# Performance work log

Hardware: AMD Instinct MI355X
Metric: run time of the kernel (lower is better)

## Reference

```python
import jax, jax.numpy as jnp
import numpy as np

ALPHA = 0.1
MARGIN = 1.0
SLOPE = 0.2  # LeakyReLU negative_slope
OFFSET = 1.0e6

def leaky(x):
    return jnp.where(x >= 0, x, SLOPE * x)

def _xavier(key, shape, gain=np.sqrt(2.0)):
    fan_out, fan_in = shape[0], shape[1]
    std = gain * np.sqrt(2.0 / (fan_in + fan_out))
    return jax.random.normal(key, shape, dtype=jnp.float32) * std

def setup_inputs() -> dict:
    key = jax.random.key(0)
    ks = jax.random.split(key, 8)
    B, F, T, D, H = 32768, 128, 32, 16, 10
    return {
        "X": jax.random.normal(ks[0], (B, F), dtype=jnp.float32),
        "affine_weights": jax.random.normal(ks[1], (T, F, D), dtype=jnp.float32),
        "W0": _xavier(ks[2], (H, D)),
        "W1": _xavier(ks[3], (H, H)),
        "W2": _xavier(ks[4], (H, H)),
        "W3": _xavier(ks[5], (H, H)),
        "Wh": _xavier(ks[6], (T, H)),
        "bh": jnp.zeros((T,), dtype=jnp.float32),
    }

def reference(X, affine_weights, W0, W1, W2, W3, Wh, bh):
    T = affine_weights.shape[0]
    # goad_transforms: x_trans [B, trans_dim, n_trans]; labels[b,t] = t (implicit)
    x_trans = jnp.einsum('bn,ant->bta', X, affine_weights)
    # ConvNet encoder, kernel_size=1 convs == per-position channel matmuls
    h = jnp.einsum('od,bdt->bot', W0, x_trans)
    for W in (W1, W2, W3):
        h = jnp.einsum('od,bdt->bot', W, leaky(h))
    rep = h                                   # [B, H, T]
    # head: LeakyReLU + Conv1d(H->T, bias=True)
    pred = jnp.einsum('oh,bht->bot', Wh, leaky(rep)) + bh[None, :, None]  # [B, T, T]
    batch_rep = jnp.transpose(rep, (0, 2, 1))  # [B, T, H]
    # CrossEntropy(reduction='none') with labels[b,t]=t -> -diag of log_softmax over class dim
    logp = jax.nn.log_softmax(pred, axis=1)
    loss_ce = -jnp.diagonal(logp, axis1=1, axis2=2)          # [B, T]
    # triplet center loss
    means = jnp.mean(batch_rep, axis=0)                       # [T, H]
    res = jnp.sum((batch_rep[:, :, None, :] - means[None, None, :, :]) ** 2, axis=-1)  # [B,T,T]
    pos = jnp.diagonal(res, axis1=1, axis2=2)                 # [B, T]
    neg = jnp.min(res + jnp.eye(T, dtype=res.dtype) * OFFSET, axis=-1)  # [B, T]
    loss_tc = jnp.mean(jnp.maximum(pos + MARGIN - neg, 0.0))  # scalar
    loss = jnp.mean(ALPHA * loss_tc + loss_ce, axis=1)        # [B]
    return batch_rep, loss
```

## Files before the change

kernel.cpp:

```cpp
#include <hip/hip_runtime.h>

typedef __attribute__((ext_vector_type(8))) short bf16x8;
typedef __attribute__((ext_vector_type(4))) float f32x4;

#define BTOT 32768
#define FDIM 128
#define TDIM 32
#define DDIM 16
#define HDIM 10
#define CDIM 320
#define ALPHA_C 0.1f
#define MARGIN_C 1.0f
#define SLOPE_C 0.2f
#define OFFSET_C 1.0e6f

#define WS_A0BF 0
#define WS_MEAN 20480
#define WS_TC   20800
#define WS_CE   20864

#define R2OFF 23552
#define LDS_TOTAL (R2OFF + 21760)
#define YSROW 92
#define MPROW 81

__device__ __forceinline__ float leaky(float x) { return fmaxf(x, SLOPE_C * x); }

__device__ __forceinline__ unsigned short f2bf(float f) {
    unsigned int u = __float_as_uint(f);
    u += 0x7fffu + ((u >> 16) & 1u);
    return (unsigned short)(u >> 16);
}

__global__ void prep_kernel(const float* __restrict__ aw, const float* __restrict__ W0,
                            unsigned short* __restrict__ a0bf) {
    int idx = blockIdx.x * blockDim.x + threadIdx.x;
    if (idx >= CDIM * FDIM) return;
    int c = idx >> 7, n = idx & 127;
    int t = c / HDIM, o = c - t * HDIM;
    const float* a = aw + ((size_t)t * FDIM + n) * DDIM;
    const float* w = W0 + o * DDIM;
    float s = 0.f;
#pragma unroll
    for (int d = 0; d < DDIM; ++d) s += a[d] * w[d];
    a0bf[idx] = f2bf(s);
}

__global__ __launch_bounds__(256, 3) void gemm0_fused(
    const float* __restrict__ X, const unsigned short* __restrict__ a0bf,
    const float* __restrict__ W1, const float* __restrict__ W2,
    const float* __restrict__ W3, const float* __restrict__ Wh,
    const float* __restrict__ bh,
    float* __restrict__ rep, float* __restrict__ ce_acc,
    float* __restrict__ mean_acc)
{
    __shared__ __align__(16) char ldsbuf[LDS_TOTAL];
    unsigned short (*xs)[136]  = (unsigned short (*)[136])ldsbuf;
    float* ysf = (float*)ldsbuf;
    unsigned short (*a0s)[136] = (unsigned short (*)[136])(ldsbuf + R2OFF);
    float* mpartf = (float*)(ldsbuf + R2OFF);

    int tid = threadIdx.x;
    int bchunk = blockIdx.x >> 2, cchunk = blockIdx.x & 3;
    int b0 = bchunk * 64, c0 = cchunk * 80;

#pragma unroll
    for (int k = 0; k < 8; ++k) {
        int idx = tid + k * 256;
        int row = idx >> 5, col4 = idx & 31;
        float4 v = reinterpret_cast<const float4*>(X + (size_t)(b0 + row) * FDIM)[col4];
        unsigned pk0, pk1;
        asm("v_cvt_pk_bf16_f32 %0, %1, %2" : "=v"(pk0) : "v"(v.x), "v"(v.y));
        asm("v_cvt_pk_bf16_f32 %0, %1, %2" : "=v"(pk1) : "v"(v.z), "v"(v.w));
        uint2 pk; pk.x = pk0; pk.y = pk1;
        *reinterpret_cast<uint2*>(&xs[row][col4 * 4]) = pk;
    }
#pragma unroll
    for (int k = 0; k < 5; ++k) {
        int idx = tid + k * 256;
        int row = idx >> 4, j = idx & 15;
        uint4 v = reinterpret_cast<const uint4*>(a0bf + (size_t)(c0 + row) * FDIM)[j];
        *reinterpret_cast<uint4*>(&a0s[row][j * 8]) = v;
    }
    __syncthreads();

    int lane = tid & 63, w = __builtin_amdgcn_readfirstlane(tid >> 6);
    int r16 = lane & 15, g = lane >> 4;
    bf16x8 af[4];
#pragma unroll
    for (int s = 0; s < 4; ++s)
        af[s] = *reinterpret_cast<const bf16x8*>(&xs[w * 16 + r16][s * 32 + g * 8]);
    __syncthreads();

#pragma unroll
    for (int ct = 0; ct < 5; ++ct) {
        f32x4 acc = {0.f, 0.f, 0.f, 0.f};
#pragma unroll
        for (int s = 0; s < 4; ++s) {
            bf16x8 bfrag = *reinterpret_cast<const bf16x8*>(&a0s[ct * 16 + r16][s * 32 + g * 8]);
            acc = __builtin_amdgcn_mfma_f32_16x16x32_bf16(af[s], bfrag, acc, 0, 0, 0);
        }
        int c = ct * 16 + r16;
        int cpad = c + c / 10;
        int ybase = (w * 16 + g * 4) * YSROW + cpad;
#pragma unroll
        for (int r = 0; r < 4; ++r) ysf[ybase + r * YSROW] = acc[r];
    }
    __syncthreads();

    int t8 = tid & 7, bl0 = tid >> 3;
    int t = cchunk * 8 + t8;
    float mgg[HDIM];
#pragma unroll
    for (int o = 0; o < HDIM; ++o) mgg[o] = 0.f;

#pragma unroll
    for (int p = 0; p < 2; ++p) {
        int bl = bl0 + p * 32;
        const float* yrow = ysf + bl * YSROW + t8 * 11;
        float h[HDIM], lh[HDIM], gg[HDIM];
#pragma unroll
        for (int q = 0; q < HDIM; ++q) h[q] = yrow[q];
#pragma unroll
        for (int o = 0; o < HDIM; ++o) lh[o] = leaky(h[o]);
#pragma unroll
        for (int o = 0; o < HDIM; ++o) { float s = 0.f;
#pragma unroll
            for (int i = 0; i < HDIM; ++i) s += W1[o * HDIM + i] * lh[i]; gg[o] = s; }
#pragma unroll
        for (int o = 0; o < HDIM; ++o) lh[o] = leaky(gg[o]);
#pragma unroll
        for (int o = 0; o < HDIM; ++o) { float s = 0.f;
#pragma unroll
            for (int i = 0; i < HDIM; ++i) s += W2[o * HDIM + i] * lh[i]; h[o] = s; }
#pragma unroll
        for (int o = 0; o < HDIM; ++o) lh[o] = leaky(h[o]);
#pragma unroll
        for (int o = 0; o < HDIM; ++o) { float s = 0.f;
#pragma unroll
            for (int i = 0; i < HDIM; ++i) s += W3[o * HDIM + i] * lh[i]; gg[o] = s; }

        float* rp = rep + (size_t)(b0 + bl) * CDIM + c0 + t8 * 10;
#pragma unroll
        for (int q = 0; q < 5; ++q) {
            float2 v; v.x = gg[2 * q]; v.y = gg[2 * q + 1];
            reinterpret_cast<float2*>(rp)[q] = v;
        }
#pragma unroll
        for (int o = 0; o < HDIM; ++o) mgg[o] += gg[o];

#pragma unroll
        for (int o = 0; o < HDIM; ++o) lh[o] = leaky(gg[o]);
        float m = -1e30f, se = 0.f, pt = 0.f;
#pragma unroll
        for (int o = 0; o < TDIM; ++o) {
            float s = bh[o];
#pragma unroll
            for (int i = 0; i < HDIM; ++i) s += Wh[o * HDIM + i] * lh[i];
            pt = (o == t) ? s : pt;
            float d = s - m;
            float e = __expf(-fabsf(d));
            float ra = d > 0.f ? e : 1.f;
            float rb = d > 0.f ? 1.f : e;
            se = se * ra + rb;
            m = fmaxf(m, s);
        }
        float ce = m + __logf(se) - pt;
        ce += __shfl_xor(ce, 1, 64);
        ce += __shfl_xor(ce, 2, 64);
        ce += __shfl_xor(ce, 4, 64);
        if (t8 == 0) atomicAdd(&ce_acc[b0 + bl], ce);
    }

#pragma unroll
    for (int o = 0; o < HDIM; ++o) mpartf[bl0 * MPROW + t8 * HDIM + o] = mgg[o];
    __syncthreads();
    if (tid < 80) {
        float s = 0.f;
#pragma unroll
        for (int r = 0; r < 32; ++r) s += mpartf[r * MPROW + tid];
        atomicAdd(&mean_acc[c0 + tid], s);
    }
}

__global__ __launch_bounds__(256) void tc_kernel(const float* __restrict__ rep,
    const float* __restrict__ mean_acc, float* __restrict__ tc_sum)
{
    __shared__ float tile[32][CDIM];
    __shared__ float mm[CDIM];
    __shared__ float msq[TDIM];
    __shared__ float wpart[4];
    int tid = threadIdx.x;
    int b0 = blockIdx.x * 32;

    for (int i = tid; i < CDIM; i += 256) mm[i] = mean_acc[i] * (1.f / BTOT);
    const float4* src = reinterpret_cast<const float4*>(rep + (size_t)b0 * CDIM);
#pragma unroll
    for (int k = 0; k < 10; ++k) {
        int idx = tid + k * 256;
        int row = idx / 80, col4 = idx - row * 80;
        *reinterpret_cast<float4*>(&tile[row][col4 * 4]) = src[idx];
    }
    __syncthreads();
    if (tid < TDIM) {
        float s = 0.f;
#pragma unroll
        for (int h = 0; h < HDIM; ++h) { float v = mm[tid * HDIM + h]; s += v * v; }
        msq[tid] = s;
    }
    __syncthreads();

    int t = tid & 31, bg = tid >> 5;
    float rv[4][HDIM], rsq[4];
#pragma unroll
    for (int j = 0; j < 4; ++j) {
        const float* rp = &tile[bg * 4 + j][t * HDIM];
        float s = 0.f;
#pragma unroll
        for (int q = 0; q < 5; ++q) {
            float2 v = reinterpret_cast<const float2*>(rp)[q];
            rv[j][2 * q] = v.x; rv[j][2 * q + 1] = v.y;
            s += v.x * v.x + v.y * v.y;
        }
        rsq[j] = s;
    }
    float pos[4], neg[4];
#pragma unroll
    for (int j = 0; j < 4; ++j) { pos[j] = 0.f; neg[j] = 1e30f; }
#pragma unroll 4
    for (int c = 0; c < TDIM; ++c) {
        float m0[HDIM];
#pragma unroll
        for (int q = 0; q < 5; ++q) {
            float2 v = reinterpret_cast<const float2*>(&mm[c * HDIM])[q];
            m0[2 * q] = v.x; m0[2 * q + 1] = v.y;
        }
        float mq = msq[c];
        bool isT = (c == t);
#pragma unroll
        for (int j = 0; j < 4; ++j) {
            float dot = 0.f;
#pragma unroll
            for (int h = 0; h < HDIM; ++h) dot += rv[j][h] * m0[h];
            float s = rsq[j] - 2.f * dot + mq;
            if (isT) pos[j] = s;
            float s2 = isT ? s + OFFSET_C : s;
            neg[j] = fminf(neg[j], s2);
        }
    }
    float hs = 0.f;
#pragma unroll
    for (int j = 0; j < 4; ++j) hs += fmaxf(pos[j] + MARGIN_C - neg[j], 0.f);
#pragma unroll
    for (int m = 1; m < 64; m <<= 1) hs += __shfl_xor(hs, m, 64);
    int lane = tid & 63, w = tid >> 6;
    if (lane == 0) wpart[w] = hs;
    __syncthreads();
    if (tid == 0) atomicAdd(tc_sum, wpart[0] + wpart[1] + wpart[2] + wpart[3]);
}

__global__ void final_kernel(const float* __restrict__ ce_acc,
                             const float* __restrict__ tc_sum, float* __restrict__ loss)
{
    int b = blockIdx.x * blockDim.x + threadIdx.x;
    if (b < BTOT)
        loss[b] = ALPHA_C * (tc_sum[0] * (1.f / ((float)BTOT * TDIM)))
                + ce_acc[b] * (1.f / TDIM);
}

extern "C" void kernel_launch(void* const* d_in, const int* in_sizes, int n_in,
                              void* d_out, int out_size, void* d_ws, size_t ws_size,
                              hipStream_t stream) {
    const float* X  = (const float*)d_in[0];
    const float* aw = (const float*)d_in[1];
    const float* W0 = (const float*)d_in[2];
    const float* W1 = (const float*)d_in[3];
    const float* W2 = (const float*)d_in[4];
    const float* W3 = (const float*)d_in[5];
    const float* Wh = (const float*)d_in[6];
    const float* bh = (const float*)d_in[7];
    float* ws = (float*)d_ws;
    unsigned short* a0bf = (unsigned short*)(ws + WS_A0BF);
    float* mean_acc = ws + WS_MEAN;
    float* tc_sum   = ws + WS_TC;
    float* ce_acc   = ws + WS_CE;
    float* out_rep = (float*)d_out;
    float* loss = out_rep + (size_t)BTOT * TDIM * HDIM;

    hipMemsetAsync(mean_acc, 0, (384 + BTOT) * sizeof(float), stream);
    prep_kernel<<<(CDIM * FDIM) / 256, 256, 0, stream>>>(aw, W0, a0bf);
    gemm0_fused<<<2048, 256, 0, stream>>>(X, a0bf, W1, W2, W3, Wh, bh,
                                          out_rep, ce_acc, mean_acc);
    tc_kernel<<<BTOT / 32, 256, 0, stream>>>(out_rep, mean_acc, tc_sum);
    final_kernel<<<BTOT / 256, 256, 0, stream>>>(ce_acc, tc_sum, loss);
}
```

Measured before the change: 90.83 us.

## Run encoder layers and head on MFMA with lane-shuffle fragment chaining

Rewrites the fused kernel so the three 10x10 encoder layers and the 32-way head run as zero-padded bf16 MFMA ops instead of scalar FMA loops. Intermediate activations are passed between MFMAs through cross-lane shuffles rather than an LDS staging tile. The A0 weight is padded to 16 outputs per transform, each block now covers 32 batch rows across all transforms, and the per-row CE atomics are replaced by one atomic per row. This targets the scalar ALU cost of the small dense layers and the LDS round trip. In exchange it computes the hidden layers in bf16, which lowers precision, and wastes MFMA work on padding.

```diff
diff --git a/kernel.cpp b/kernel.cpp
--- a/kernel.cpp
+++ b/kernel.cpp
@@ -14,15 +14,10 @@
 #define SLOPE_C 0.2f
 #define OFFSET_C 1.0e6f
 
-#define WS_A0BF 0
-#define WS_MEAN 20480
-#define WS_TC   20800
-#define WS_CE   20864
-
-#define R2OFF 23552
-#define LDS_TOTAL (R2OFF + 21760)
-#define YSROW 92
-#define MPROW 81
+#define WS_A0P  0
+#define WS_MEAN 32768
+#define WS_TC   33088
+#define WS_CE   33152
 
 __device__ __forceinline__ float leaky(float x) { return fmaxf(x, SLOPE_C * x); }
 
@@ -32,154 +27,184 @@
     return (unsigned short)(u >> 16);
 }
 
+__device__ __forceinline__ f32x4 mfma32(bf16x8 a, bf16x8 b, f32x4 c) {
+    return __builtin_amdgcn_mfma_f32_16x16x32_bf16(a, b, c, 0, 0, 0);
+}
+
+__device__ __forceinline__ void leaky_pack(f32x4 v, unsigned& p0, unsigned& p1) {
+    float a0 = leaky(v[0]), a1 = leaky(v[1]), a2 = leaky(v[2]), a3 = leaky(v[3]);
+    asm("v_cvt_pk_bf16_f32 %0, %1, %2" : "=v"(p0) : "v"(a0), "v"(a1));
+    asm("v_cvt_pk_bf16_f32 %0, %1, %2" : "=v"(p1) : "v"(a2), "v"(a3));
+}
+
+__device__ __forceinline__ bf16x8 build_bfrag(unsigned p0, unsigned p1, int g, int r16) {
+    int s0 = ((2 * g) * 16 + r16) & 63;
+    int s1 = ((2 * g + 1) * 16 + r16) & 63;
+    unsigned w0 = (unsigned)__shfl((int)p0, s0, 64);
+    unsigned w1 = (unsigned)__shfl((int)p1, s0, 64);
+    unsigned w2 = (unsigned)__shfl((int)p0, s1, 64);
+    unsigned w3 = (unsigned)__shfl((int)p1, s1, 64);
+    unsigned zm = (g < 2) ? 0xFFFFFFFFu : 0u;
+    union { unsigned u[4]; bf16x8 v; } r;
+    r.u[0] = w0 & zm; r.u[1] = w1 & zm; r.u[2] = w2 & zm; r.u[3] = w3 & zm;
+    return r.v;
+}
+
 __global__ void prep_kernel(const float* __restrict__ aw, const float* __restrict__ W0,
-                            unsigned short* __restrict__ a0bf) {
+                            unsigned short* __restrict__ a0p) {
     int idx = blockIdx.x * blockDim.x + threadIdx.x;
-    if (idx >= CDIM * FDIM) return;
-    int c = idx >> 7, n = idx & 127;
-    int t = c / HDIM, o = c - t * HDIM;
-    const float* a = aw + ((size_t)t * FDIM + n) * DDIM;
-    const float* w = W0 + o * DDIM;
-    float s = 0.f;
-#pragma unroll
-    for (int d = 0; d < DDIM; ++d) s += a[d] * w[d];
-    a0bf[idx] = f2bf(s);
-}
-
-__global__ __launch_bounds__(256, 3) void gemm0_fused(
-    const float* __restrict__ X, const unsigned short* __restrict__ a0bf,
+    if (idx >= 65536) return;
+    int n = idx & 127, o = (idx >> 7) & 15, t = idx >> 11;
+    unsigned short r = 0;
+    if (o < 10) {
+        const float* a = aw + ((size_t)t * FDIM + n) * DDIM;
+        const float* w = W0 + o * DDIM;
+        float s = 0.f;
+#pragma unroll
+        for (int d = 0; d < DDIM; ++d) s += a[d] * w[d];
+        r = f2bf(s);
+    }
+    a0p[idx] = r;
+}
+
+__global__ __launch_bounds__(256, 4) void gemm0_fused(
+    const float* __restrict__ X, const unsigned short* __restrict__ a0p,
     const float* __restrict__ W1, const float* __restrict__ W2,
     const float* __restrict__ W3, const float* __restrict__ Wh,
     const float* __restrict__ bh,
     float* __restrict__ rep, float* __restrict__ ce_acc,
     float* __restrict__ mean_acc)
 {
-    __shared__ __align__(16) char ldsbuf[LDS_TOTAL];
-    unsigned short (*xs)[136]  = (unsigned short (*)[136])ldsbuf;
-    float* ysf = (float*)ldsbuf;
-    unsigned short (*a0s)[136] = (unsigned short (*)[136])(ldsbuf + R2OFF);
-    float* mpartf = (float*)(ldsbuf + R2OFF);
+    __shared__ unsigned short xs[32][136];
+    __shared__ unsigned short w1x[16][32], w2x[16][32], w3x[16][32], whx[32][32];
+    __shared__ float mred[2][32][12];
 
     int tid = threadIdx.x;
-    int bchunk = blockIdx.x >> 2, cchunk = blockIdx.x & 3;
-    int b0 = bchunk * 64, c0 = cchunk * 80;
-
-#pragma unroll
-    for (int k = 0; k < 8; ++k) {
+    int b0 = blockIdx.x * 32;
+
+#pragma unroll
+    for (int k = 0; k < 4; ++k) {
         int idx = tid + k * 256;
         int row = idx >> 5, col4 = idx & 31;
         float4 v = reinterpret_cast<const float4*>(X + (size_t)(b0 + row) * FDIM)[col4];
-        unsigned pk0, pk1;
-        asm("v_cvt_pk_bf16_f32 %0, %1, %2" : "=v"(pk0) : "v"(v.x), "v"(v.y));
-        asm("v_cvt_pk_bf16_f32 %0, %1, %2" : "=v"(pk1) : "v"(v.z), "v"(v.w));
-        uint2 pk; pk.x = pk0; pk.y = pk1;
+        unsigned p0, p1;
+        asm("v_cvt_pk_bf16_f32 %0, %1, %2" : "=v"(p0) : "v"(v.x), "v"(v.y));
+        asm("v_cvt_pk_bf16_f32 %0, %1, %2" : "=v"(p1) : "v"(v.z), "v"(v.w));
+        uint2 pk; pk.x = p0; pk.y = p1;
         *reinterpret_cast<uint2*>(&xs[row][col4 * 4]) = pk;
     }
 #pragma unroll
-    for (int k = 0; k < 5; ++k) {
-        int idx = tid + k * 256;
-        int row = idx >> 4, j = idx & 15;
-        uint4 v = reinterpret_cast<const uint4*>(a0bf + (size_t)(c0 + row) * FDIM)[j];
-        *reinterpret_cast<uint4*>(&a0s[row][j * 8]) = v;
+    for (int k = 0; k < 2; ++k) {
+        int i = tid + k * 256;
+        int o = i >> 5, kk = i & 31;
+        bool in10 = (o < 10 && kk < 10);
+        w1x[o][kk] = in10 ? f2bf(W1[o * 10 + kk]) : (unsigned short)0;
+        w2x[o][kk] = in10 ? f2bf(W2[o * 10 + kk]) : (unsigned short)0;
+        w3x[o][kk] = in10 ? f2bf(W3[o * 10 + kk]) : (unsigned short)0;
+    }
+#pragma unroll
+    for (int k = 0; k < 4; ++k) {
+        int i = tid + k * 256;
+        int o = i >> 5, kk = i & 31;
+        whx[o][kk] = (kk < 10) ? f2bf(Wh[o * 10 + kk]) : (unsigned short)0;
     }
     __syncthreads();
 
     int lane = tid & 63, w = __builtin_amdgcn_readfirstlane(tid >> 6);
     int r16 = lane & 15, g = lane >> 4;
-    bf16x8 af[4];
+    int bsub = w >> 1, thalf = w & 1;
+    int bglob = b0 + bsub * 16 + r16;
+
+    bf16x8 xf[4];
 #pragma unroll
     for (int s = 0; s < 4; ++s)
-        af[s] = *reinterpret_cast<const bf16x8*>(&xs[w * 16 + r16][s * 32 + g * 8]);
-    __syncthreads();
-
-#pragma unroll
-    for (int ct = 0; ct < 5; ++ct) {
-        f32x4 acc = {0.f, 0.f, 0.f, 0.f};
-#pragma unroll
-        for (int s = 0; s < 4; ++s) {
-            bf16x8 bfrag = *reinterpret_cast<const bf16x8*>(&a0s[ct * 16 + r16][s * 32 + g * 8]);
-            acc = __builtin_amdgcn_mfma_f32_16x16x32_bf16(af[s], bfrag, acc, 0, 0, 0);
+        xf[s] = *reinterpret_cast<const bf16x8*>(&xs[bsub * 16 + r16][s * 32 + g * 8]);
+
+    bf16x8 w1f = *reinterpret_cast<const bf16x8*>(&w1x[r16][g * 8]);
+    bf16x8 w2f = *reinterpret_cast<const bf16x8*>(&w2x[r16][g * 8]);
+    bf16x8 w3f = *reinterpret_cast<const bf16x8*>(&w3x[r16][g * 8]);
+    bf16x8 whAf = *reinterpret_cast<const bf16x8*>(&whx[r16][g * 8]);
+    bf16x8 whBf = *reinterpret_cast<const bf16x8*>(&whx[16 + r16][g * 8]);
+    f32x4 bhA, bhB;
+#pragma unroll
+    for (int r = 0; r < 4; ++r) { bhA[r] = bh[g * 4 + r]; bhB[r] = bh[16 + g * 4 + r]; }
+    const f32x4 zero4 = {0.f, 0.f, 0.f, 0.f};
+
+    float ce_local = 0.f;
+
+    for (int tt4 = 0; tt4 < 4; ++tt4) {
+#pragma unroll
+        for (int q = 0; q < 4; ++q) {
+            int t = thalf * 16 + tt4 * 4 + q;
+            const bf16x8* ap = reinterpret_cast<const bf16x8*>(
+                a0p + ((size_t)t * 16 + r16) * 128);
+            f32x4 acc = zero4;
+#pragma unroll
+            for (int s = 0; s < 4; ++s)
+                acc = mfma32(ap[s * 4 + g], xf[s], acc);
+
+            unsigned p0, p1;
+            leaky_pack(acc, p0, p1);
+            bf16x8 bf = build_bfrag(p0, p1, g, r16);
+            f32x4 d1 = mfma32(w1f, bf, zero4);
+            leaky_pack(d1, p0, p1);
+            bf = build_bfrag(p0, p1, g, r16);
+            f32x4 d2 = mfma32(w2f, bf, zero4);
+            leaky_pack(d2, p0, p1);
+            bf = build_bfrag(p0, p1, g, r16);
+            f32x4 d3 = mfma32(w3f, bf, zero4);
+
+            float* rp = rep + (size_t)bglob * CDIM + t * HDIM + g * 4;
+            if (g < 2) {
+                float2 v0; v0.x = d3[0]; v0.y = d3[1];
+                float2 v1; v1.x = d3[2]; v1.y = d3[3];
+                reinterpret_cast<float2*>(rp)[0] = v0;
+                reinterpret_cast<float2*>(rp)[1] = v1;
+            } else if (g == 2) {
+                float2 v0; v0.x = d3[0]; v0.y = d3[1];
+                reinterpret_cast<float2*>(rp)[0] = v0;
+            }
+
+            float m0 = d3[0], m1 = d3[1], m2 = d3[2], m3 = d3[3];
+#pragma unroll
+            for (int msk = 1; msk < 16; msk <<= 1) {
+                m0 += __shfl_xor(m0, msk, 64);
+                m1 += __shfl_xor(m1, msk, 64);
+                m2 += __shfl_xor(m2, msk, 64);
+                m3 += __shfl_xor(m3, msk, 64);
+            }
+            if (r16 == 0 && g < 3) {
+                float4 mv; mv.x = m0; mv.y = m1; mv.z = m2; mv.w = m3;
+                *reinterpret_cast<float4*>(&mred[bsub][t][g * 4]) = mv;
+            }
+
+            leaky_pack(d3, p0, p1);
+            bf = build_bfrag(p0, p1, g, r16);
+            f32x4 pA = mfma32(whAf, bf, bhA);
+            f32x4 pB = mfma32(whBf, bf, bhB);
+
+            float mx = fmaxf(fmaxf(fmaxf(pA[0], pA[1]), fmaxf(pA[2], pA[3])),
+                             fmaxf(fmaxf(pB[0], pB[1]), fmaxf(pB[2], pB[3])));
+            mx = fmaxf(mx, __shfl_xor(mx, 16, 64));
+            mx = fmaxf(mx, __shfl_xor(mx, 32, 64));
+            float se = __expf(pA[0] - mx) + __expf(pA[1] - mx) +
+                       __expf(pA[2] - mx) + __expf(pA[3] - mx) +
+                       __expf(pB[0] - mx) + __expf(pB[1] - mx) +
+                       __expf(pB[2] - mx) + __expf(pB[3] - mx);
+            se += __shfl_xor(se, 16, 64);
+            se += __shfl_xor(se, 32, 64);
+            float lse = mx + __logf(se);
+            float pr = thalf ? pB[q] : pA[q];
+            float ptv = __shfl(pr, tt4 * 16 + r16, 64);
+            ce_local += lse - ptv;
         }
-        int c = ct * 16 + r16;
-        int cpad = c + c / 10;
-        int ybase = (w * 16 + g * 4) * YSROW + cpad;
-#pragma unroll
-        for (int r = 0; r < 4; ++r) ysf[ybase + r * YSROW] = acc[r];
-    }
-    __syncthreads();
-
-    int t8 = tid & 7, bl0 = tid >> 3;
-    int t = cchunk * 8 + t8;
-    float mgg[HDIM];
-#pragma unroll
-    for (int o = 0; o < HDIM; ++o) mgg[o] = 0.f;
-
-#pragma unroll
-    for (int p = 0; p < 2; ++p) {
-        int bl = bl0 + p * 32;
-        const float* yrow = ysf + bl * YSROW + t8 * 11;
-        float h[HDIM], lh[HDIM], gg[HDIM];
-#pragma unroll
-        for (int q = 0; q < HDIM; ++q) h[q] = yrow[q];
-#pragma unroll
-        for (int o = 0; o < HDIM; ++o) lh[o] = leaky(h[o]);
-#pragma unroll
-        for (int o = 0; o < HDIM; ++o) { float s = 0.f;
-#pragma unroll
-            for (int i = 0; i < HDIM; ++i) s += W1[o * HDIM + i] * lh[i]; gg[o] = s; }
-#pragma unroll
-        for (int o = 0; o < HDIM; ++o) lh[o] = leaky(gg[o]);
-#pragma unroll
-        for (int o = 0; o < HDIM; ++o) { float s = 0.f;
-#pragma unroll
-            for (int i = 0; i < HDIM; ++i) s += W2[o * HDIM + i] * lh[i]; h[o] = s; }
-#pragma unroll
-        for (int o = 0; o < HDIM; ++o) lh[o] = leaky(h[o]);
-#pragma unroll
-        for (int o = 0; o < HDIM; ++o) { float s = 0.f;
-#pragma unroll
-            for (int i = 0; i < HDIM; ++i) s += W3[o * HDIM + i] * lh[i]; gg[o] = s; }
-
-        float* rp = rep + (size_t)(b0 + bl) * CDIM + c0 + t8 * 10;
-#pragma unroll
-        for (int q = 0; q < 5; ++q) {
-            float2 v; v.x = gg[2 * q]; v.y = gg[2 * q + 1];
-            reinterpret_cast<float2*>(rp)[q] = v;
-        }
-#pragma unroll
-        for (int o = 0; o < HDIM; ++o) mgg[o] += gg[o];
-
-#pragma unroll
-        for (int o = 0; o < HDIM; ++o) lh[o] = leaky(gg[o]);
-        float m = -1e30f, se = 0.f, pt = 0.f;
-#pragma unroll
-        for (int o = 0; o < TDIM; ++o) {
-            float s = bh[o];
-#pragma unroll
-            for (int i = 0; i < HDIM; ++i) s += Wh[o * HDIM + i] * lh[i];
-            pt = (o == t) ? s : pt;
-            float d = s - m;
-            float e = __expf(-fabsf(d));
-            float ra = d > 0.f ? e : 1.f;
-            float rb = d > 0.f ? 1.f : e;
-            se = se * ra + rb;
-            m = fmaxf(m, s);
-        }
-        float ce = m + __logf(se) - pt;
-        ce += __shfl_xor(ce, 1, 64);
-        ce += __shfl_xor(ce, 2, 64);
-        ce += __shfl_xor(ce, 4, 64);
-        if (t8 == 0) atomicAdd(&ce_acc[b0 + bl], ce);
-    }
-
-#pragma unroll
-    for (int o = 0; o < HDIM; ++o) mpartf[bl0 * MPROW + t8 * HDIM + o] = mgg[o];
-    __syncthreads();
-    if (tid < 80) {
-        float s = 0.f;
-#pragma unroll
-        for (int r = 0; r < 32; ++r) s += mpartf[r * MPROW + tid];
-        atomicAdd(&mean_acc[c0 + tid], s);
+    }
+
+    if (g == 0) atomicAdd(&ce_acc[bglob], ce_local);
+    __syncthreads();
+    for (int i = tid; i < TDIM * HDIM; i += 256) {
+        int t = i / 10, o = i - t * 10;
+        atomicAdd(&mean_acc[i], mred[0][t][o] + mred[1][t][o]);
     }
 }
 
@@ -280,7 +305,7 @@
     const float* Wh = (const float*)d_in[6];
     const float* bh = (const float*)d_in[7];
     float* ws = (float*)d_ws;
-    unsigned short* a0bf = (unsigned short*)(ws + WS_A0BF);
+    unsigned short* a0p = (unsigned short*)(ws + WS_A0P);
     float* mean_acc = ws + WS_MEAN;
     float* tc_sum   = ws + WS_TC;
     float* ce_acc   = ws + WS_CE;
@@ -288,9 +313,9 @@
     float* loss = out_rep + (size_t)BTOT * TDIM * HDIM;
 
     hipMemsetAsync(mean_acc, 0, (384 + BTOT) * sizeof(float), stream);
-    prep_kernel<<<(CDIM * FDIM) / 256, 256, 0, stream>>>(aw, W0, a0bf);
-    gemm0_fused<<<2048, 256, 0, stream>>>(X, a0bf, W1, W2, W3, Wh, bh,
-                                          out_rep, ce_acc, mean_acc);
+    prep_kernel<<<256, 256, 0, stream>>>(aw, W0, a0p);
+    gemm0_fused<<<BTOT / 32, 256, 0, stream>>>(X, a0p, W1, W2, W3, Wh, bh,
+                                               out_rep, ce_acc, mean_acc);
     tc_kernel<<<BTOT / 32, 256, 0, stream>>>(out_rep, mean_acc, tc_sum);
     final_kernel<<<BTOT / 256, 256, 0, stream>>>(ce_acc, tc_sum, loss);
 }
```

After: 102.9 us. 13.3% more time.

## Move CE head into tc kernel, split mean reduction, restructure gemm0 tiling

Applied to the files above, without the earlier changes.

The classification head and cross-entropy move out of the gemm0 kernel into the triplet-center kernel, which already holds rep in LDS. The CE sums are then written directly per sample, so the atomics and the large memset go away. The column mean is now computed by a separate kernel that rereads rep. Gemm0 now uses 32-row blocks over half the transforms each, reads padded A0 fragments straight from global memory instead of staging them in LDS, and raises occupancy to 4 blocks per CU. The cost is an extra pass over rep for the mean and more global loads of A0.

```diff
diff --git a/kernel.cpp b/kernel.cpp
--- a/kernel.cpp
+++ b/kernel.cpp
@@ -14,15 +14,12 @@
 #define SLOPE_C 0.2f
 #define OFFSET_C 1.0e6f
 
-#define WS_A0BF 0
-#define WS_MEAN 20480
-#define WS_TC   20800
-#define WS_CE   20864
-
-#define R2OFF 23552
-#define LDS_TOTAL (R2OFF + 21760)
-#define YSROW 92
-#define MPROW 81
+#define WS_A0P  0
+#define WS_MEAN 32768
+#define WS_TC   33088
+#define WS_CE   33152
+
+#define YSROW 163
 
 __device__ __forceinline__ float leaky(float x) { return fmaxf(x, SLOPE_C * x); }
 
@@ -32,95 +29,96 @@
     return (unsigned short)(u >> 16);
 }
 
+__device__ __forceinline__ f32x4 mfma32(bf16x8 a, bf16x8 b, f32x4 c) {
+    return __builtin_amdgcn_mfma_f32_16x16x32_bf16(a, b, c, 0, 0, 0);
+}
+
 __global__ void prep_kernel(const float* __restrict__ aw, const float* __restrict__ W0,
-                            unsigned short* __restrict__ a0bf) {
+                            unsigned short* __restrict__ a0p) {
     int idx = blockIdx.x * blockDim.x + threadIdx.x;
-    if (idx >= CDIM * FDIM) return;
-    int c = idx >> 7, n = idx & 127;
-    int t = c / HDIM, o = c - t * HDIM;
-    const float* a = aw + ((size_t)t * FDIM + n) * DDIM;
-    const float* w = W0 + o * DDIM;
-    float s = 0.f;
-#pragma unroll
-    for (int d = 0; d < DDIM; ++d) s += a[d] * w[d];
-    a0bf[idx] = f2bf(s);
-}
-
-__global__ __launch_bounds__(256, 3) void gemm0_fused(
-    const float* __restrict__ X, const unsigned short* __restrict__ a0bf,
+    if (idx >= 65536) return;
+    int n = idx & 127, o = (idx >> 7) & 15, t = idx >> 11;
+    unsigned short r = 0;
+    if (o < 10) {
+        const float* a = aw + ((size_t)t * FDIM + n) * DDIM;
+        const float* w = W0 + o * DDIM;
+        float s = 0.f;
+#pragma unroll
+        for (int d = 0; d < DDIM; ++d) s += a[d] * w[d];
+        r = f2bf(s);
+    }
+    a0p[idx] = r;
+}
+
+__global__ __launch_bounds__(256, 4) void gemm0_fused(
+    const float* __restrict__ X, const unsigned short* __restrict__ a0p,
     const float* __restrict__ W1, const float* __restrict__ W2,
-    const float* __restrict__ W3, const float* __restrict__ Wh,
-    const float* __restrict__ bh,
-    float* __restrict__ rep, float* __restrict__ ce_acc,
-    float* __restrict__ mean_acc)
+    const float* __restrict__ W3,
+    float* __restrict__ rep)
 {
-    __shared__ __align__(16) char ldsbuf[LDS_TOTAL];
-    unsigned short (*xs)[136]  = (unsigned short (*)[136])ldsbuf;
+    __shared__ __align__(16) char ldsbuf[32 * YSROW * 4];
+    unsigned short (*xs)[136] = (unsigned short (*)[136])ldsbuf;
     float* ysf = (float*)ldsbuf;
-    unsigned short (*a0s)[136] = (unsigned short (*)[136])(ldsbuf + R2OFF);
-    float* mpartf = (float*)(ldsbuf + R2OFF);
 
     int tid = threadIdx.x;
-    int bchunk = blockIdx.x >> 2, cchunk = blockIdx.x & 3;
-    int b0 = bchunk * 64, c0 = cchunk * 80;
-
-#pragma unroll
-    for (int k = 0; k < 8; ++k) {
+    int b0 = (blockIdx.x >> 1) * 32;
+    int thalf = blockIdx.x & 1;
+
+#pragma unroll
+    for (int k = 0; k < 4; ++k) {
         int idx = tid + k * 256;
         int row = idx >> 5, col4 = idx & 31;
         float4 v = reinterpret_cast<const float4*>(X + (size_t)(b0 + row) * FDIM)[col4];
-        unsigned pk0, pk1;
-        asm("v_cvt_pk_bf16_f32 %0, %1, %2" : "=v"(pk0) : "v"(v.x), "v"(v.y));
-        asm("v_cvt_pk_bf16_f32 %0, %1, %2" : "=v"(pk1) : "v"(v.z), "v"(v.w));
-        uint2 pk; pk.x = pk0; pk.y = pk1;
+        unsigned p0, p1;
+        asm("v_cvt_pk_bf16_f32 %0, %1, %2" : "=v"(p0) : "v"(v.x), "v"(v.y));
+        asm("v_cvt_pk_bf16_f32 %0, %1, %2" : "=v"(p1) : "v"(v.z), "v"(v.w));
+        uint2 pk; pk.x = p0; pk.y = p1;
         *reinterpret_cast<uint2*>(&xs[row][col4 * 4]) = pk;
-    }
-#pragma unroll
-    for (int k = 0; k < 5; ++k) {
-        int idx = tid + k * 256;
-        int row = idx >> 4, j = idx & 15;
-        uint4 v = reinterpret_cast<const uint4*>(a0bf + (size_t)(c0 + row) * FDIM)[j];
-        *reinterpret_cast<uint4*>(&a0s[row][j * 8]) = v;
     }
     __syncthreads();
 
     int lane = tid & 63, w = __builtin_amdgcn_readfirstlane(tid >> 6);
     int r16 = lane & 15, g = lane >> 4;
-    bf16x8 af[4];
+    int bsub = w >> 1, tq = w & 1;
+
+    bf16x8 xf[4];
 #pragma unroll
     for (int s = 0; s < 4; ++s)
-        af[s] = *reinterpret_cast<const bf16x8*>(&xs[w * 16 + r16][s * 32 + g * 8]);
-    __syncthreads();
-
-#pragma unroll
-    for (int ct = 0; ct < 5; ++ct) {
-        f32x4 acc = {0.f, 0.f, 0.f, 0.f};
-#pragma unroll
-        for (int s = 0; s < 4; ++s) {
-            bf16x8 bfrag = *reinterpret_cast<const bf16x8*>(&a0s[ct * 16 + r16][s * 32 + g * 8]);
-            acc = __builtin_amdgcn_mfma_f32_16x16x32_bf16(af[s], bfrag, acc, 0, 0, 0);
-        }
-        int c = ct * 16 + r16;
-        int cpad = c + c / 10;
-        int ybase = (w * 16 + g * 4) * YSROW + cpad;
-#pragma unroll
-        for (int r = 0; r < 4; ++r) ysf[ybase + r * YSROW] = acc[r];
-    }
-    __syncthreads();
-
-    int t8 = tid & 7, bl0 = tid >> 3;
-    int t = cchunk * 8 + t8;
-    float mgg[HDIM];
-#pragma unroll
-    for (int o = 0; o < HDIM; ++o) mgg[o] = 0.f;
-
+        xf[s] = *reinterpret_cast<const bf16x8*>(&xs[bsub * 16 + r16][s * 32 + g * 8]);
+    __syncthreads();
+
+    int rowb = (bsub * 16 + r16) * YSROW;
+#pragma unroll
+    for (int tt = 0; tt < 8; ++tt) {
+        int t = thalf * 16 + tq * 8 + tt;
+        const bf16x8* ap = reinterpret_cast<const bf16x8*>(
+            a0p + ((size_t)t * 16 + r16) * 128);
+        f32x4 a0 = {0.f, 0.f, 0.f, 0.f}, a1 = {0.f, 0.f, 0.f, 0.f};
+        a0 = mfma32(ap[0 * 4 + g], xf[0], a0);
+        a1 = mfma32(ap[1 * 4 + g], xf[1], a1);
+        a0 = mfma32(ap[2 * 4 + g], xf[2], a0);
+        a1 = mfma32(ap[3 * 4 + g], xf[3], a1);
+        int colb = (tq * 8 + tt) * 10 + g * 4;
+        if (g < 2) {
+            ysf[rowb + colb + 0] = a0[0] + a1[0];
+            ysf[rowb + colb + 1] = a0[1] + a1[1];
+            ysf[rowb + colb + 2] = a0[2] + a1[2];
+            ysf[rowb + colb + 3] = a0[3] + a1[3];
+        } else if (g == 2) {
+            ysf[rowb + colb + 0] = a0[0] + a1[0];
+            ysf[rowb + colb + 1] = a0[1] + a1[1];
+        }
+    }
+    __syncthreads();
+
+    int bl = tid >> 3, t8 = tid & 7;
 #pragma unroll
     for (int p = 0; p < 2; ++p) {
-        int bl = bl0 + p * 32;
-        const float* yrow = ysf + bl * YSROW + t8 * 11;
+        int tloc = t8 + p * 8;
+        const float* yrow = ysf + bl * YSROW + tloc * 10;
         float h[HDIM], lh[HDIM], gg[HDIM];
 #pragma unroll
-        for (int q = 0; q < HDIM; ++q) h[q] = yrow[q];
+        for (int o = 0; o < HDIM; ++o) h[o] = yrow[o];
 #pragma unroll
         for (int o = 0; o < HDIM; ++o) lh[o] = leaky(h[o]);
 #pragma unroll
@@ -140,55 +138,38 @@
 #pragma unroll
             for (int i = 0; i < HDIM; ++i) s += W3[o * HDIM + i] * lh[i]; gg[o] = s; }
 
-        float* rp = rep + (size_t)(b0 + bl) * CDIM + c0 + t8 * 10;
+        float* rp = rep + (size_t)(b0 + bl) * CDIM + (thalf * 16 + tloc) * HDIM;
 #pragma unroll
         for (int q = 0; q < 5; ++q) {
             float2 v; v.x = gg[2 * q]; v.y = gg[2 * q + 1];
             reinterpret_cast<float2*>(rp)[q] = v;
         }
-#pragma unroll
-        for (int o = 0; o < HDIM; ++o) mgg[o] += gg[o];
-
-#pragma unroll
-        for (int o = 0; o < HDIM; ++o) lh[o] = leaky(gg[o]);
-        float m = -1e30f, se = 0.f, pt = 0.f;
-#pragma unroll
-        for (int o = 0; o < TDIM; ++o) {
-            float s = bh[o];
-#pragma unroll
-            for (int i = 0; i < HDIM; ++i) s += Wh[o * HDIM + i] * lh[i];
-            pt = (o == t) ? s : pt;
-            float d = s - m;
-            float e = __expf(-fabsf(d));
-            float ra = d > 0.f ? e : 1.f;
-            float rb = d > 0.f ? 1.f : e;
-            se = se * ra + rb;
-            m = fmaxf(m, s);
-        }
-        float ce = m + __logf(se) - pt;
-        ce += __shfl_xor(ce, 1, 64);
-        ce += __shfl_xor(ce, 2, 64);
-        ce += __shfl_xor(ce, 4, 64);
-        if (t8 == 0) atomicAdd(&ce_acc[b0 + bl], ce);
-    }
-
-#pragma unroll
-    for (int o = 0; o < HDIM; ++o) mpartf[bl0 * MPROW + t8 * HDIM + o] = mgg[o];
-    __syncthreads();
-    if (tid < 80) {
-        float s = 0.f;
-#pragma unroll
-        for (int r = 0; r < 32; ++r) s += mpartf[r * MPROW + tid];
-        atomicAdd(&mean_acc[c0 + tid], s);
-    }
-}
-
-__global__ __launch_bounds__(256) void tc_kernel(const float* __restrict__ rep,
-    const float* __restrict__ mean_acc, float* __restrict__ tc_sum)
+    }
+}
+
+__global__ void meanred_kernel(const float* __restrict__ rep, float* __restrict__ mean_acc)
+{
+    int j = threadIdx.x;
+    const float* base = rep + (size_t)blockIdx.x * 128 * CDIM;
+    float s0 = 0, s1 = 0, s2 = 0, s3 = 0;
+    for (int b = 0; b < 128; b += 4) {
+        s0 += base[(size_t)(b + 0) * CDIM + j];
+        s1 += base[(size_t)(b + 1) * CDIM + j];
+        s2 += base[(size_t)(b + 2) * CDIM + j];
+        s3 += base[(size_t)(b + 3) * CDIM + j];
+    }
+    atomicAdd(&mean_acc[j], s0 + s1 + s2 + s3);
+}
+
+__global__ __launch_bounds__(256) void tc_head_kernel(const float* __restrict__ rep,
+    const float* __restrict__ mean_acc,
+    const float* __restrict__ Wh, const float* __restrict__ bh,
+    float* __restrict__ tc_sum, float* __restrict__ ce_out)
 {
     __shared__ float tile[32][CDIM];
     __shared__ float mm[CDIM];
     __shared__ float msq[TDIM];
+    __shared__ float cep[32][33];
     __shared__ float wpart[4];
     int tid = threadIdx.x;
     int b0 = blockIdx.x * 32;
@@ -224,6 +205,7 @@
         }
         rsq[j] = s;
     }
+
     float pos[4], neg[4];
 #pragma unroll
     for (int j = 0; j < 4; ++j) { pos[j] = 0.f; neg[j] = 1e30f; }
@@ -255,17 +237,42 @@
     for (int m = 1; m < 64; m <<= 1) hs += __shfl_xor(hs, m, 64);
     int lane = tid & 63, w = tid >> 6;
     if (lane == 0) wpart[w] = hs;
-    __syncthreads();
+
+#pragma unroll
+    for (int j = 0; j < 4; ++j) {
+        float lh[HDIM];
+#pragma unroll
+        for (int o = 0; o < HDIM; ++o) lh[o] = leaky(rv[j][o]);
+        float m = -1e30f, se = 0.f, pt = 0.f;
+#pragma unroll
+        for (int o = 0; o < TDIM; ++o) {
+            float s = bh[o];
+#pragma unroll
+            for (int i = 0; i < HDIM; ++i) s += Wh[o * HDIM + i] * lh[i];
+            pt = (o == t) ? s : pt;
+            float d = s - m;
+            float e = __expf(-fabsf(d));
+            se = (d > 0.f) ? se * e + 1.f : se + e;
+            m = fmaxf(m, s);
+        }
+        cep[bg * 4 + j][t] = m + __logf(se) - pt;
+    }
+    __syncthreads();
+    if (tid < 32) {
+        float s = 0.f;
+#pragma unroll
+        for (int k = 0; k < 32; ++k) s += cep[tid][k];
+        ce_out[b0 + tid] = s * (1.f / TDIM);
+    }
     if (tid == 0) atomicAdd(tc_sum, wpart[0] + wpart[1] + wpart[2] + wpart[3]);
 }
 
-__global__ void final_kernel(const float* __restrict__ ce_acc,
+__global__ void final_kernel(const float* __restrict__ ce_out,
                              const float* __restrict__ tc_sum, float* __restrict__ loss)
 {
     int b = blockIdx.x * blockDim.x + threadIdx.x;
     if (b < BTOT)
-        loss[b] = ALPHA_C * (tc_sum[0] * (1.f / ((float)BTOT * TDIM)))
-                + ce_acc[b] * (1.f / TDIM);
+        loss[b] = ALPHA_C * (tc_sum[0] * (1.f / ((float)BTOT * TDIM))) + ce_out[b];
 }
 
 extern "C" void kernel_launch(void* const* d_in, const int* in_sizes, int n_in,
@@ -280,17 +287,18 @@
     const float* Wh = (const float*)d_in[6];
     const float* bh = (const float*)d_in[7];
     float* ws = (float*)d_ws;
-    unsigned short* a0bf = (unsigned short*)(ws + WS_A0BF);
+    unsigned short* a0p = (unsigned short*)(ws + WS_A0P);
     float* mean_acc = ws + WS_MEAN;
     float* tc_sum   = ws + WS_TC;
-    float* ce_acc   = ws + WS_CE;
+    float* ce_out   = ws + WS_CE;
     float* out_rep = (float*)d_out;
     float* loss = out_rep + (size_t)BTOT * TDIM * HDIM;
 
-    hipMemsetAsync(mean_acc, 0, (384 + BTOT) * sizeof(float), stream);
-    prep_kernel<<<(CDIM * FDIM) / 256, 256, 0, stream>>>(aw, W0, a0bf);
-    gemm0_fused<<<2048, 256, 0, stream>>>(X, a0bf, W1, W2, W3, Wh, bh,
-                                          out_rep, ce_acc, mean_acc);
-    tc_kernel<<<BTOT / 32, 256, 0, stream>>>(out_rep, mean_acc, tc_sum);
-    final_kernel<<<BTOT / 256, 256, 0, stream>>>(ce_acc, tc_sum, loss);
-}
+    hipMemsetAsync(mean_acc, 0, 384 * sizeof(float), stream);
+    prep_kernel<<<256, 256, 0, stream>>>(aw, W0, a0p);
+    gemm0_fused<<<2048, 256, 0, stream>>>(X, a0p, W1, W2, W3, out_rep);
+    meanred_kernel<<<256, 320, 0, stream>>>(out_rep, mean_acc);
+    tc_head_kernel<<<BTOT / 32, 256, 0, stream>>>(out_rep, mean_acc, Wh, bh,
+                                                  tc_sum, ce_out);
+    final_kernel<<<BTOT / 256, 256, 0, stream>>>(ce_out, tc_sum, loss);
+}
```

Result: slower. 179.6 us (+97.7%).
